# Performance work log

Measured on AMD Instinct MI355X. Metric: run time of the kernel, lower is better.

Reference implementation:

```python
import jax, jax.numpy as jnp
import numpy as np

BLOCK_SIZE = 128


def setup_inputs() -> dict:
    key = jax.random.key(0)
    kq, kk, kv = jax.random.split(key, 3)
    b, t, e = 16, 8192, 256
    Q = jax.random.normal(kq, (b, t, e), dtype=jnp.float32)
    K = jax.random.normal(kk, (b, t, e), dtype=jnp.float32)
    V = jax.random.normal(kv, (b, t, e), dtype=jnp.float32)
    return {"Q": Q, "K": K, "V": V}


def reference(Q, K, V):
    b, t, e = Q.shape
    bs = BLOCK_SIZE
    n = t // bs
    scale = 1.0 / jnp.sqrt(jnp.asarray(e, Q.dtype))
    Qb = Q.reshape(b, n, bs, e)
    Kb = K.reshape(b, n, bs, e)
    Vb = V.reshape(b, n, bs, e)
    # block-diagonal scores: [b, n, bs, bs]
    Z = jnp.einsum('bnqe,bnke->bnqk', Qb, Kb) * scale
    causal = jnp.triu(jnp.ones((bs, bs), dtype=bool), k=1)  # True above diagonal
    Z = jnp.where(causal, -jnp.inf, Z)
    A = jax.nn.softmax(Z, axis=-1)
    out = jnp.einsum('bnqk,bnke->bnqe', A, Vb).reshape(b, t, e)
    A_flat = A.reshape(b, t, bs)  # matches torch view(b, t, block_size)
    return out, A_flat
```

## Files before the change

kernel.cpp:

```cpp
#include <hip/hip_runtime.h>

#define T_  8192
#define E_  256
#define BS_ 128

typedef __attribute__((ext_vector_type(8))) short bf16x8;
typedef __attribute__((ext_vector_type(4))) float f32x4;
typedef __attribute__((ext_vector_type(4))) unsigned int u32x4;

__device__ __forceinline__ unsigned pkbf(float a, float b) {
    unsigned short ua = __builtin_bit_cast(unsigned short, (__bf16)a);
    unsigned short ub = __builtin_bit_cast(unsigned short, (__bf16)b);
    return (unsigned)ua | ((unsigned)ub << 16);
}

__device__ __forceinline__ unsigned short bf1(float a) {
    return __builtin_bit_cast(unsigned short, (__bf16)a);
}

__device__ __forceinline__ bf16x8 pack8(f32x4 a, f32x4 b) {
    u32x4 u;
    u[0] = pkbf(a[0], a[1]); u[1] = pkbf(a[2], a[3]);
    u[2] = pkbf(b[0], b[1]); u[3] = pkbf(b[2], b[3]);
    return __builtin_bit_cast(bf16x8, u);
}

__device__ __forceinline__ void lds_barrier() {
    asm volatile("s_waitcnt lgkmcnt(0)" ::: "memory");
    __builtin_amdgcn_s_barrier();
}

__global__ __launch_bounds__(512, 4) void dba_fused(
        const float* __restrict__ Qg, const float* __restrict__ Kg,
        const float* __restrict__ Vg, float* __restrict__ Ag,
        float* __restrict__ Og)
{
    __shared__ unsigned short Sm[BS_ * E_];

    const int tid  = threadIdx.x;
    const int lane = tid & 63;
    const int w    = tid >> 6;
    const int cl   = lane & 15;
    const int g    = lane >> 4;
    const int bi   = blockIdx.x >> 6;
    const int ni   = blockIdx.x & 63;
    const int base  = (bi * T_ + ni * BS_) * E_;
    const int abase = (bi * T_ + ni * BS_) * BS_;
    const int vcol  = w * 32 + cl;

    const float* qp = Qg + base + (w * 16 + cl) * E_;
    f32x4 q0 = __builtin_nontemporal_load((const f32x4*)(qp + g * 8));
    f32x4 q1 = __builtin_nontemporal_load((const f32x4*)(qp + g * 8 + 4));

    {
        const int c4   = lane * 4;
        const int chnk = c4 >> 3;
        const int klow = c4 & 7;
        #pragma unroll 8
        for (int i = 0; i < 16; ++i) {
            const int n = i * 8 + w;
            f32x4 kv = __builtin_nontemporal_load((const f32x4*)(Kg + base + n * E_ + c4));
            const int cp = chnk ^ (n & 15);
            uint2 pk;
            pk.x = pkbf(kv[0], kv[1]);
            pk.y = pkbf(kv[2], kv[3]);
            *(uint2*)&Sm[n * E_ + cp * 8 + klow] = pk;
        }
    }
    lds_barrier();

    f32x4 acc[8];
    #pragma unroll
    for (int nt = 0; nt < 8; ++nt) acc[nt] = (f32x4){0.f, 0.f, 0.f, 0.f};

    for (int ks = 0; ks < 8; ++ks) {
        bf16x8 aq = pack8(q0, q1);
        if (ks < 7) {
            const int kn = (ks + 1) * 32 + g * 8;
            q0 = __builtin_nontemporal_load((const f32x4*)(qp + kn));
            q1 = __builtin_nontemporal_load((const f32x4*)(qp + kn + 4));
        }
        #pragma unroll
        for (int nt = 0; nt < 8; ++nt) {
            const int n  = nt * 16 + cl;
            const int cp = (ks * 4 + g) ^ cl;
            bf16x8 bk = *(const bf16x8*)&Sm[n * E_ + cp * 8];
            acc[nt] = __builtin_amdgcn_mfma_f32_16x16x32_bf16(aq, bk, acc[nt], 0, 0, 0);
        }
    }

    float vb[2][16];
    #pragma unroll
    for (int t = 0; t < 16; ++t)
        vb[0][t] = __builtin_nontemporal_load(
            Vg + base + (g * 8 + (t & 7)) * E_ + vcol + (t >> 3) * 16);
    #pragma unroll
    for (int t = 0; t < 16; ++t)
        vb[1][t] = __builtin_nontemporal_load(
            Vg + base + (32 + g * 8 + (t & 7)) * E_ + vcol + (t >> 3) * 16);

    const float scale = 0.0625f;
    const float L2E   = 1.4426950408889634f;
    #pragma unroll
    for (int r = 0; r < 4; ++r) {
        const int q = w * 16 + g * 4 + r;
        float m = -__builtin_inff();
        #pragma unroll
        for (int nt = 0; nt < 8; ++nt) {
            const int c = nt * 16 + cl;
            float z = acc[nt][r] * scale;
            z = (c > q) ? -__builtin_inff() : z;
            acc[nt][r] = z;
            m = fmaxf(m, z);
        }
        m = fmaxf(m, __shfl_xor(m, 1));
        m = fmaxf(m, __shfl_xor(m, 2));
        m = fmaxf(m, __shfl_xor(m, 4));
        m = fmaxf(m, __shfl_xor(m, 8));
        float s = 0.f;
        #pragma unroll
        for (int nt = 0; nt < 8; ++nt) {
            const float p = exp2f((acc[nt][r] - m) * L2E);
            acc[nt][r] = p;
            s += p;
        }
        s += __shfl_xor(s, 1);
        s += __shfl_xor(s, 2);
        s += __shfl_xor(s, 4);
        s += __shfl_xor(s, 8);
        const float rinv = __builtin_amdgcn_rcpf(s);
        #pragma unroll
        for (int nt = 0; nt < 8; ++nt)
            acc[nt][r] *= rinv;
    }

    #pragma unroll
    for (int nt = 0; nt < 8; ++nt)
        #pragma unroll
        for (int r = 0; r < 4; ++r)
            __builtin_nontemporal_store(acc[nt][r],
                Ag + abase + (w * 16 + g * 4 + r) * BS_ + nt * 16 + cl);

    lds_barrier();

    #pragma unroll
    for (int nt = 0; nt < 8; ++nt)
        #pragma unroll
        for (int r = 0; r < 4; ++r) {
            const int q = w * 16 + g * 4 + r;
            const int k = nt * 16 + cl;
            Sm[q * BS_ + (((k >> 3) ^ (g * 4 + r)) * 8) + (k & 7)] = bf1(acc[nt][r]);
        }

    lds_barrier();

    f32x4 acc2[8][2];
    #pragma unroll
    for (int mt = 0; mt < 8; ++mt) {
        acc2[mt][0] = (f32x4){0.f, 0.f, 0.f, 0.f};
        acc2[mt][1] = (f32x4){0.f, 0.f, 0.f, 0.f};
    }

    #pragma unroll
    for (int ks = 0; ks < 4; ++ks) {
        f32x4 v0a = {vb[ks & 1][0],  vb[ks & 1][1],  vb[ks & 1][2],  vb[ks & 1][3]};
        f32x4 v0b = {vb[ks & 1][4],  vb[ks & 1][5],  vb[ks & 1][6],  vb[ks & 1][7]};
        f32x4 v1a = {vb[ks & 1][8],  vb[ks & 1][9],  vb[ks & 1][10], vb[ks & 1][11]};
        f32x4 v1b = {vb[ks & 1][12], vb[ks & 1][13], vb[ks & 1][14], vb[ks & 1][15]};
        bf16x8 bv0 = pack8(v0a, v0b);
        bf16x8 bv1 = pack8(v1a, v1b);
        if (ks < 2) {
            #pragma unroll
            for (int t = 0; t < 16; ++t)
                vb[ks & 1][t] = __builtin_nontemporal_load(
                    Vg + base + ((ks + 2) * 32 + g * 8 + (t & 7)) * E_ + vcol + (t >> 3) * 16);
        }
        #pragma unroll
        for (int mt = 0; mt < 8; ++mt) {
            const int q = mt * 16 + cl;
            const bf16x8 pa = *(const bf16x8*)&Sm[q * BS_ + (((ks * 4 + g) ^ cl) * 8)];
            acc2[mt][0] = __builtin_amdgcn_mfma_f32_16x16x32_bf16(pa, bv0, acc2[mt][0], 0, 0, 0);
            acc2[mt][1] = __builtin_amdgcn_mfma_f32_16x16x32_bf16(pa, bv1, acc2[mt][1], 0, 0, 0);
        }
    }

    #pragma unroll
    for (int mt = 0; mt < 8; ++mt)
        #pragma unroll
        for (int n2 = 0; n2 < 2; ++n2)
            #pragma unroll
            for (int r = 0; r < 4; ++r)
                __builtin_nontemporal_store(acc2[mt][n2][r],
                    Og + base + (mt * 16 + g * 4 + r) * E_ + vcol + n2 * 16);
}

extern "C" void kernel_launch(void* const* d_in, const int* in_sizes, int n_in,
                              void* d_out, int out_size, void* d_ws, size_t ws_size,
                              hipStream_t stream) {
    const float* Q = (const float*)d_in[0];
    const float* K = (const float*)d_in[1];
    const float* V = (const float*)d_in[2];
    float* O = (float*)d_out;
    const int b = in_sizes[0] / (T_ * E_);
    float* A = O + (size_t)b * T_ * E_;
    dim3 grid(b * (T_ / BS_));
    dim3 block(512);
    dba_fused<<<grid, block, 0, stream>>>(Q, K, V, A, O);
}
```

Baseline: 448.8 us.

## Load K directly into MFMA registers instead of staging through LDS

Drops the cooperative K staging into shared memory and its barrier. Each wave now loads K straight from global memory in the MFMA B-operand layout, using a 4-slot register prefetch ring that is converted to bf16 just before each MFMA. This shrinks LDS to the 128x128 probability buffer, which could allow more resident blocks and removes one sync. The cost is that every wave reads the whole K block, so K traffic to L2 is duplicated eightfold, and register pressure rises.

```diff
diff --git a/kernel.cpp b/kernel.cpp
--- a/kernel.cpp
+++ b/kernel.cpp
@@ -35,7 +35,7 @@
         const float* __restrict__ Vg, float* __restrict__ Ag,
         float* __restrict__ Og)
 {
-    __shared__ unsigned short Sm[BS_ * E_];
+    __shared__ unsigned short Sm[BS_ * BS_];
 
     const int tid  = threadIdx.x;
     const int lane = tid & 63;
@@ -52,27 +52,20 @@
     f32x4 q0 = __builtin_nontemporal_load((const f32x4*)(qp + g * 8));
     f32x4 q1 = __builtin_nontemporal_load((const f32x4*)(qp + g * 8 + 4));
 
-    {
-        const int c4   = lane * 4;
-        const int chnk = c4 >> 3;
-        const int klow = c4 & 7;
-        #pragma unroll 8
-        for (int i = 0; i < 16; ++i) {
-            const int n = i * 8 + w;
-            f32x4 kv = __builtin_nontemporal_load((const f32x4*)(Kg + base + n * E_ + c4));
-            const int cp = chnk ^ (n & 15);
-            uint2 pk;
-            pk.x = pkbf(kv[0], kv[1]);
-            pk.y = pkbf(kv[2], kv[3]);
-            *(uint2*)&Sm[n * E_ + cp * 8 + klow] = pk;
-        }
-    }
-    lds_barrier();
+    const float* kp = Kg + base + cl * E_ + g * 8;
+
+    f32x4 kb[4][2];
+    #pragma unroll
+    for (int i = 0; i < 4; ++i) {
+        kb[i][0] = __builtin_nontemporal_load((const f32x4*)(kp + i * 16 * E_));
+        kb[i][1] = __builtin_nontemporal_load((const f32x4*)(kp + i * 16 * E_ + 4));
+    }
 
     f32x4 acc[8];
     #pragma unroll
     for (int nt = 0; nt < 8; ++nt) acc[nt] = (f32x4){0.f, 0.f, 0.f, 0.f};
 
+    #pragma unroll
     for (int ks = 0; ks < 8; ++ks) {
         bf16x8 aq = pack8(q0, q1);
         if (ks < 7) {
@@ -82,9 +75,17 @@
         }
         #pragma unroll
         for (int nt = 0; nt < 8; ++nt) {
-            const int n  = nt * 16 + cl;
-            const int cp = (ks * 4 + g) ^ cl;
-            bf16x8 bk = *(const bf16x8*)&Sm[n * E_ + cp * 8];
+            const int slot = nt & 3;
+            bf16x8 bk = pack8(kb[slot][0], kb[slot][1]);
+            const int pn  = nt + 4;
+            const int pks = ks + (pn >> 3);
+            const int pnt = pn & 7;
+            if (pks < 8) {
+                kb[slot][0] = __builtin_nontemporal_load(
+                    (const f32x4*)(kp + pnt * 16 * E_ + pks * 32));
+                kb[slot][1] = __builtin_nontemporal_load(
+                    (const f32x4*)(kp + pnt * 16 * E_ + pks * 32 + 4));
+            }
             acc[nt] = __builtin_amdgcn_mfma_f32_16x16x32_bf16(aq, bk, acc[nt], 0, 0, 0);
         }
     }
@@ -140,8 +141,6 @@
         for (int r = 0; r < 4; ++r)
             __builtin_nontemporal_store(acc[nt][r],
                 Ag + abase + (w * 16 + g * 4 + r) * BS_ + nt * 16 + cl);
-
-    lds_barrier();
 
     #pragma unroll
     for (int nt = 0; nt < 8; ++nt)
```

Result: slower. 609.3 us (+35.8%).
